# Performance work log

Measured on AMD Instinct MI355X. Metric: run time of the kernel, lower is better.

Reference implementation:

```python
import jax, jax.numpy as jnp
import numpy as np

D_MODEL = 1024
NUM_HEADS = 16
D_K = D_MODEL // NUM_HEADS  # 64
THETA = 10000.0


def setup_inputs() -> dict:
    key = jax.random.key(0)
    k_x, k_q, k_k, k_v, k_o = jax.random.split(key, 5)
    B, S = 2, 2048
    std = (2.0 / (D_MODEL + D_MODEL)) ** 0.5
    x = jax.random.normal(k_x, (B, S, D_MODEL), dtype=jnp.float32)
    Wq = std * jax.random.truncated_normal(k_q, -3.0, 3.0, (D_MODEL, D_MODEL), dtype=jnp.float32)
    Wk = std * jax.random.truncated_normal(k_k, -3.0, 3.0, (D_MODEL, D_MODEL), dtype=jnp.float32)
    Wv = std * jax.random.truncated_normal(k_v, -3.0, 3.0, (D_MODEL, D_MODEL), dtype=jnp.float32)
    Wo = std * jax.random.truncated_normal(k_o, -3.0, 3.0, (D_MODEL, D_MODEL), dtype=jnp.float32)
    return {"x": x, "Wq": Wq, "Wk": Wk, "Wv": Wv, "Wo": Wo}


def _apply_rope(t, cos, sin):
    # t: [B, H, S, d_k]; cos/sin: [S, d_k//2] broadcast over B, H
    tr = t.reshape(*t.shape[:-1], D_K // 2, 2)
    t1, t2 = tr[..., 0], tr[..., 1]
    r1 = t1 * cos - t2 * sin
    r2 = t1 * sin + t2 * cos
    return jnp.stack([r1, r2], axis=-1).reshape(t.shape)


def reference(x, Wq, Wk, Wv, Wo):
    B, S, D = x.shape
    H, dk = NUM_HEADS, D_K
    # projections (no bias): y = x @ W.T
    Q = (x @ Wq.T).reshape(B, S, H, dk).transpose(0, 2, 1, 3)  # [B,H,S,dk]
    K = (x @ Wk.T).reshape(B, S, H, dk).transpose(0, 2, 1, 3)
    V = (x @ Wv.T).reshape(B, S, H, dk).transpose(0, 2, 1, 3)
    # RoPE angles for positions 0..S-1
    pos = jnp.arange(S, dtype=jnp.float32)[:, None]            # [S,1]
    freqs = 1.0 / (THETA ** (jnp.arange(0, dk, 2, dtype=jnp.float32) / dk))  # [dk/2]
    angles = pos * freqs[None, :]                              # [S, dk/2]
    cos, sin = jnp.cos(angles), jnp.sin(angles)
    Q = _apply_rope(Q, cos, sin)
    K = _apply_rope(K, cos, sin)
    # causal scaled dot-product attention
    scores = jnp.einsum("bhqd,bhkd->bhqk", Q, K) / jnp.sqrt(jnp.float32(dk))
    causal = jnp.tril(jnp.ones((S, S), dtype=bool))
    scores = jnp.where(causal, scores, -jnp.inf)
    probs = jax.nn.softmax(scores, axis=-1)
    attn = jnp.einsum("bhqk,bhkd->bhqd", probs, V)             # [B,H,S,dk]
    attn = attn.transpose(0, 2, 1, 3).reshape(B, S, H * dk)
    return attn @ Wo.T
```

## Files before the change

### kernel.cpp

```cpp
#include <hip/hip_runtime.h>
#include <hip/hip_bf16.h>

typedef __bf16 bf16;
typedef __bf16 bf16x8 __attribute__((ext_vector_type(8)));
typedef float f32x4 __attribute__((ext_vector_type(4)));

#define MFMA16(A, B, C) __builtin_amdgcn_mfma_f32_16x16x32_bf16((A), (B), (C), 0, 0, 0)

static __device__ __forceinline__ void gload16(const bf16* g, bf16* l) {
    __builtin_amdgcn_global_load_lds((const __attribute__((address_space(1))) void*)g,
                                     (__attribute__((address_space(3))) void*)l, 16, 0, 0);
}

__global__ void detect_kernel(const void* w, int* flag) {
    float v = (float)((const bf16*)w)[threadIdx.x];
    unsigned long long bad = __ballot(!(fabsf(v) < 1.0f));
    if (threadIdx.x == 0) *flag = bad ? 1 : 0;
}

__global__ __launch_bounds__(256) void convert_all(const void* x, const void* w0,
                                                   const void* w1, const void* w2,
                                                   const void* w3, bf16* xb, bf16* b0,
                                                   bf16* b1, bf16* b2, bf16* b3,
                                                   const int* flagp) {
    if (*flagp == 0) return;
    int id = (blockIdx.x * 256 + threadIdx.x) * 4;
    const int XN = 1 << 22;
    const float* src;
    bf16* dst;
    int off;
    if (id < XN) {
        src = (const float*)x; dst = xb; off = id;
    } else {
        int r = id - XN;
        int wi = r >> 20;
        off = r & ((1 << 20) - 1);
        src = (const float*)(wi == 0 ? w0 : wi == 1 ? w1 : wi == 2 ? w2 : w3);
        dst = (wi == 0 ? b0 : wi == 1 ? b1 : wi == 2 ? b2 : b3);
    }
    float4 v = *(const float4*)(src + off);
    bf16 o[4] = {(bf16)v.x, (bf16)v.y, (bf16)v.z, (bf16)v.w};
    *(uint2*)(dst + off) = *(uint2*)o;
}

__global__ __launch_bounds__(128) void gemm_qkv(const void* rawA, const bf16* convA,
                                                const void* rWq, const bf16* cWq,
                                                const void* rWk, const bf16* cWk,
                                                const void* rWv, const bf16* cWv,
                                                bf16* Qo, bf16* Ko, bf16* Vt,
                                                const int* flagp) {
    const int K = 1024;
    __shared__ __attribute__((aligned(16))) bf16 lsA[128 * 64];
    __shared__ __attribute__((aligned(16))) bf16 lsB[64 * 64];
    const int flag = *flagp;
    const bf16* A = flag ? convA : (const bf16*)rawA;
    const int tensor = blockIdx.x >> 4;
    const int n0 = (blockIdx.x & 15) * 64;
    const bf16* W = tensor == 0 ? (flag ? cWq : (const bf16*)rWq)
                  : tensor == 1 ? (flag ? cWk : (const bf16*)rWk)
                                : (flag ? cWv : (const bf16*)rWv);
    const int t = threadIdx.x;
    const int m0 = blockIdx.y * 128;
    const int w = t >> 6, lane = t & 63;
    const int llo = lane & 15, quad = lane >> 4;
    const int srow = t >> 3;
    const int sc = (t & 7) ^ (srow & 7);
    const bf16* Ab = A + (size_t)(m0 + srow) * K + sc * 8;
    const bf16* Wb = W + (size_t)(n0 + srow) * K + sc * 8;
    bf16* lA = &lsA[t * 8];
    bf16* lB = &lsB[t * 8];

    f32x4 acc[4][4] = {};

    for (int k0 = 0; k0 < K; k0 += 64) {
#pragma unroll
        for (int j = 0; j < 8; ++j) gload16(Ab + (size_t)j * 16 * K + k0, lA + j * 1024);
#pragma unroll
        for (int j = 0; j < 4; ++j) gload16(Wb + (size_t)j * 16 * K + k0, lB + j * 1024);
        __syncthreads();
#pragma unroll
        for (int kc = 0; kc < 2; ++kc) {
            bf16x8 a[4], bb[4];
            const int g = kc * 4 + quad;
#pragma unroll
            for (int mi = 0; mi < 4; ++mi) {
                int r = w * 64 + mi * 16 + llo;
                a[mi] = *(const bf16x8*)&lsA[r * 64 + ((g ^ (r & 7)) * 8)];
            }
#pragma unroll
            for (int ni = 0; ni < 4; ++ni) {
                int r = ni * 16 + llo;
                bb[ni] = *(const bf16x8*)&lsB[r * 64 + ((g ^ (r & 7)) * 8)];
            }
#pragma unroll
            for (int mi = 0; mi < 4; ++mi)
#pragma unroll
                for (int ni = 0; ni < 4; ++ni)
                    acc[mi][ni] = MFMA16(a[mi], bb[ni], acc[mi][ni]);
        }
        __syncthreads();
    }

#pragma unroll
    for (int mi = 0; mi < 4; ++mi)
#pragma unroll
        for (int ni = 0; ni < 4; ++ni)
#pragma unroll
            for (int r = 0; r < 4; ++r) {
                int row = m0 + w * 64 + mi * 16 + quad * 4 + r;
                int col = n0 + ni * 16 + llo;
                float v = acc[mi][ni][r];
                if (tensor == 2) {
                    int b = row >> 11, s = row & 2047;
                    Vt[((size_t)b * 1024 + col) * 2048 + s] = (bf16)v;
                } else {
                    int d = col & 63, s = row & 2047;
                    float partner = __shfl_xor(v, 1);
                    float freq = exp2f((float)(d >> 1) * -0.4152410118609203f);
                    float rev = (float)s * freq * 0.15915494309189535f;
                    rev -= floorf(rev);
                    float sn = __builtin_amdgcn_sinf(rev);
                    float cs = __builtin_amdgcn_cosf(rev);
                    float outv = v * cs + partner * sn * ((d & 1) ? 1.0f : -1.0f);
                    bf16* dst = (tensor == 0) ? Qo : Ko;
                    dst[(size_t)row * 1024 + col] = (bf16)outv;
                }
            }
}

__global__ __launch_bounds__(128) void gemm_out(const bf16* A, const void* rW,
                                                const bf16* cW, void* Cout,
                                                const int* flagp) {
    const int K = 1024, N = 1024;
    __shared__ __attribute__((aligned(16))) bf16 lsA[128 * 64];
    __shared__ __attribute__((aligned(16))) bf16 lsB[64 * 64];
    const int flag = *flagp;
    const bf16* W = flag ? cW : (const bf16*)rW;
    const int t = threadIdx.x;
    const int m0 = blockIdx.y * 128;
    const int n0 = blockIdx.x * 64;
    const int w = t >> 6, lane = t & 63;
    const int llo = lane & 15, quad = lane >> 4;
    const int srow = t >> 3;
    const int sc = (t & 7) ^ (srow & 7);
    const bf16* Ab = A + (size_t)(m0 + srow) * K + sc * 8;
    const bf16* Wb = W + (size_t)(n0 + srow) * K + sc * 8;
    bf16* lA = &lsA[t * 8];
    bf16* lB = &lsB[t * 8];

    f32x4 acc[4][4] = {};

    for (int k0 = 0; k0 < K; k0 += 64) {
#pragma unroll
        for (int j = 0; j < 8; ++j) gload16(Ab + (size_t)j * 16 * K + k0, lA + j * 1024);
#pragma unroll
        for (int j = 0; j < 4; ++j) gload16(Wb + (size_t)j * 16 * K + k0, lB + j * 1024);
        __syncthreads();
#pragma unroll
        for (int kc = 0; kc < 2; ++kc) {
            bf16x8 a[4], bb[4];
            const int g = kc * 4 + quad;
#pragma unroll
            for (int mi = 0; mi < 4; ++mi) {
                int r = w * 64 + mi * 16 + llo;
                a[mi] = *(const bf16x8*)&lsA[r * 64 + ((g ^ (r & 7)) * 8)];
            }
#pragma unroll
            for (int ni = 0; ni < 4; ++ni) {
                int r = ni * 16 + llo;
                bb[ni] = *(const bf16x8*)&lsB[r * 64 + ((g ^ (r & 7)) * 8)];
            }
#pragma unroll
            for (int mi = 0; mi < 4; ++mi)
#pragma unroll
                for (int ni = 0; ni < 4; ++ni)
                    acc[mi][ni] = MFMA16(a[mi], bb[ni], acc[mi][ni]);
        }
        __syncthreads();
    }

#pragma unroll
    for (int mi = 0; mi < 4; ++mi)
#pragma unroll
        for (int ni = 0; ni < 4; ++ni)
#pragma unroll
            for (int r = 0; r < 4; ++r) {
                int row = m0 + w * 64 + mi * 16 + quad * 4 + r;
                int col = n0 + ni * 16 + llo;
                float v = acc[mi][ni][r];
                if (flag)
                    ((float*)Cout)[(size_t)row * N + col] = v;
                else
                    ((bf16*)Cout)[(size_t)row * N + col] = (bf16)v;
            }
}

__global__ __launch_bounds__(256) void attn_kernel(const bf16* __restrict__ Q,
                                                   const bf16* __restrict__ Kr,
                                                   const bf16* __restrict__ Vt,
                                                   bf16* __restrict__ O) {
    __shared__ __attribute__((aligned(16))) bf16 lsK[64 * 64];
    __shared__ __attribute__((aligned(16))) bf16 lsV[64 * 64];
    __shared__ __attribute__((aligned(16))) bf16 lsP[4][16 * 72];
    const int blk = blockIdx.x;
    const int ib = 31 - (blk >> 5);
    const int bh = blk & 31;
    const int b = bh >> 4, h = bh & 15;
    const int t = threadIdx.x, w = t >> 6, lane = t & 63;
    const int llo = lane & 15, quad = lane >> 4;
    const int q0 = ib * 64 + w * 16;

    const size_t qbase = ((size_t)(b * 2048 + q0 + llo)) * 1024 + h * 64 + quad * 8;
    bf16x8 aQ0 = *(const bf16x8*)&Q[qbase];
    bf16x8 aQ1 = *(const bf16x8*)&Q[qbase + 32];

    f32x4 o[4] = {};
    float lpart[4] = {0.f, 0.f, 0.f, 0.f};
    const float SC = 0.18033688011112042f;
    const int qrow = q0 + quad * 4;

    const int srow8 = lane >> 3;
    const int sc = (lane & 7) ^ srow8;

    for (int tt = 0; tt <= ib; ++tt) {
        const int kv0 = tt * 64;
#pragma unroll
        for (int jj = 0; jj < 2; ++jj) {
            int seg = w + jj * 4;
            int rowk = seg * 8 + srow8;
            gload16(&Kr[((size_t)(b * 2048 + kv0 + rowk)) * 1024 + h * 64 + sc * 8],
                    &lsK[seg * 512 + lane * 8]);
            gload16(&Vt[((size_t)(b * 1024 + h * 64 + rowk)) * 2048 + kv0 + sc * 8],
                    &lsV[seg * 512 + lane * 8]);
        }
        __syncthreads();
        f32x4 s[4];
#pragma unroll
        for (int half = 0; half < 4; ++half) {
            int rk = half * 16 + llo;
            bf16x8 k0 = *(const bf16x8*)&lsK[rk * 64 + ((quad ^ (rk & 7)) * 8)];
            bf16x8 k1 = *(const bf16x8*)&lsK[rk * 64 + (((quad + 4) ^ (rk & 7)) * 8)];
            f32x4 z = {};
            z = MFMA16(aQ0, k0, z);
            z = MFMA16(aQ1, k1, z);
            s[half] = z;
        }
        if (tt == ib) {
#pragma unroll
            for (int half = 0; half < 4; ++half) {
                int kv = kv0 + half * 16 + llo;
#pragma unroll
                for (int r = 0; r < 4; ++r) {
                    float e = (kv <= qrow + r) ? s[half][r] * SC : -INFINITY;
                    float p = exp2f(e);
                    lpart[r] += p;
                    lsP[w][(quad * 4 + r) * 72 + half * 16 + llo] = (bf16)p;
                }
            }
        } else {
#pragma unroll
            for (int half = 0; half < 4; ++half)
#pragma unroll
                for (int r = 0; r < 4; ++r) {
                    float p = exp2f(s[half][r] * SC);
                    lpart[r] += p;
                    lsP[w][(quad * 4 + r) * 72 + half * 16 + llo] = (bf16)p;
                }
        }
        __builtin_amdgcn_wave_barrier();
#pragma unroll
        for (int kc = 0; kc < 2; ++kc) {
            bf16x8 aP = *(const bf16x8*)&lsP[w][llo * 72 + kc * 32 + quad * 8];
#pragma unroll
            for (int g = 0; g < 4; ++g) {
                int rv = g * 16 + llo;
                int cg = kc * 4 + quad;
                bf16x8 bV = *(const bf16x8*)&lsV[rv * 64 + ((cg ^ (rv & 7)) * 8)];
                o[g] = MFMA16(aP, bV, o[g]);
            }
        }
        __syncthreads();
    }

#pragma unroll
    for (int r = 0; r < 4; ++r) {
        float l = lpart[r];
#pragma unroll
        for (int off = 1; off < 16; off <<= 1) l += __shfl_xor(l, off);
        float inv = 1.f / l;
        size_t ob = ((size_t)(b * 2048 + q0 + quad * 4 + r)) * 1024 + h * 64;
#pragma unroll
        for (int g = 0; g < 4; ++g) O[ob + g * 16 + llo] = (bf16)(o[g][r] * inv);
    }
}

extern "C" void kernel_launch(void* const* d_in, const int* in_sizes, int n_in,
                              void* d_out, int out_size, void* d_ws, size_t ws_size,
                              hipStream_t stream) {
    const size_t TN = (size_t)4096 * 1024;

    int* flag = (int*)d_ws;
    bf16* Q = (bf16*)((char*)d_ws + 256);
    bf16* Kb = Q + TN;
    bf16* Vt = Kb + TN;
    bf16* xb = Vt + TN;
    bf16* Wb0 = xb + TN;
    bf16* Wb1 = Wb0 + TN / 4;
    bf16* Wb2 = Wb1 + TN / 4;
    bf16* Wb3 = Wb2 + TN / 4;
    bf16* AO = Q;

    detect_kernel<<<1, 64, 0, stream>>>(d_in[1], flag);
    convert_all<<<8192, 256, 0, stream>>>(d_in[0], d_in[1], d_in[2], d_in[3], d_in[4],
                                          xb, Wb0, Wb1, Wb2, Wb3, flag);

    gemm_qkv<<<dim3(48, 32), 128, 0, stream>>>(d_in[0], xb, d_in[1], Wb0, d_in[2], Wb1,
                                               d_in[3], Wb2, Q, Kb, Vt, flag);

    attn_kernel<<<1024, 256, 0, stream>>>(Q, Kb, Vt, AO);

    gemm_out<<<dim3(16, 32), 128, 0, stream>>>(AO, d_in[4], Wb3, d_out, flag);
}
```

Measured before the change: 209.8 us.

## Enlarge GEMM tiles to 128x128 and give attention waves 32 query rows

The QKV and output projections now share one templated GEMM using 128x128 tiles with four waves, halving the number of B-tile loads per output. The attention kernel processes 128 queries per block (32 per wave), computing scores in transposed form and storing probabilities with packed writes, and skips fully-masked KV chunks per wave. This raises operand reuse from LDS for K/V but halves the block counts, which can reduce occupancy and increase causal load imbalance.

New measurement: 227.9 us. 1.09x slower.

```diff
diff --git a/kernel.cpp b/kernel.cpp
--- a/kernel.cpp
+++ b/kernel.cpp
@@ -43,26 +43,37 @@
     *(uint2*)(dst + off) = *(uint2*)o;
 }
 
-__global__ __launch_bounds__(128) void gemm_qkv(const void* rawA, const bf16* convA,
-                                                const void* rWq, const bf16* cWq,
-                                                const void* rWk, const bf16* cWk,
-                                                const void* rWv, const bf16* cWv,
-                                                bf16* Qo, bf16* Ko, bf16* Vt,
-                                                const int* flagp) {
+template <int MODE>
+__global__ __launch_bounds__(256) void gemm128(const void* rawA, const bf16* convA,
+                                               const void* rW0, const bf16* cW0,
+                                               const void* rW1, const bf16* cW1,
+                                               const void* rW2, const bf16* cW2,
+                                               bf16* Qo, bf16* Ko, bf16* Vt,
+                                               void* Cout, const int* flagp) {
     const int K = 1024;
     __shared__ __attribute__((aligned(16))) bf16 lsA[128 * 64];
-    __shared__ __attribute__((aligned(16))) bf16 lsB[64 * 64];
+    __shared__ __attribute__((aligned(16))) bf16 lsB[128 * 64];
     const int flag = *flagp;
     const bf16* A = flag ? convA : (const bf16*)rawA;
-    const int tensor = blockIdx.x >> 4;
-    const int n0 = (blockIdx.x & 15) * 64;
-    const bf16* W = tensor == 0 ? (flag ? cWq : (const bf16*)rWq)
-                  : tensor == 1 ? (flag ? cWk : (const bf16*)rWk)
-                                : (flag ? cWv : (const bf16*)rWv);
+    int tensor, n0;
+    const bf16* W;
+    if (MODE == 0) {
+        tensor = blockIdx.x >> 3;
+        n0 = (blockIdx.x & 7) * 128;
+        W = tensor == 0 ? (flag ? cW0 : (const bf16*)rW0)
+          : tensor == 1 ? (flag ? cW1 : (const bf16*)rW1)
+                        : (flag ? cW2 : (const bf16*)rW2);
+    } else {
+        tensor = 0;
+        n0 = blockIdx.x * 128;
+        W = flag ? cW0 : (const bf16*)rW0;
+    }
     const int t = threadIdx.x;
     const int m0 = blockIdx.y * 128;
     const int w = t >> 6, lane = t & 63;
+    const int wr = w >> 1, wc = w & 1;
     const int llo = lane & 15, quad = lane >> 4;
+
     const int srow = t >> 3;
     const int sc = (t & 7) ^ (srow & 7);
     const bf16* Ab = A + (size_t)(m0 + srow) * K + sc * 8;
@@ -74,9 +85,9 @@
 
     for (int k0 = 0; k0 < K; k0 += 64) {
 #pragma unroll
-        for (int j = 0; j < 8; ++j) gload16(Ab + (size_t)j * 16 * K + k0, lA + j * 1024);
-#pragma unroll
-        for (int j = 0; j < 4; ++j) gload16(Wb + (size_t)j * 16 * K + k0, lB + j * 1024);
+        for (int j = 0; j < 4; ++j) gload16(Ab + (size_t)j * 32 * K + k0, lA + j * 2048);
+#pragma unroll
+        for (int j = 0; j < 4; ++j) gload16(Wb + (size_t)j * 32 * K + k0, lB + j * 2048);
         __syncthreads();
 #pragma unroll
         for (int kc = 0; kc < 2; ++kc) {
@@ -84,12 +95,12 @@
             const int g = kc * 4 + quad;
 #pragma unroll
             for (int mi = 0; mi < 4; ++mi) {
-                int r = w * 64 + mi * 16 + llo;
+                int r = wr * 64 + mi * 16 + llo;
                 a[mi] = *(const bf16x8*)&lsA[r * 64 + ((g ^ (r & 7)) * 8)];
             }
 #pragma unroll
             for (int ni = 0; ni < 4; ++ni) {
-                int r = ni * 16 + llo;
+                int r = wc * 64 + ni * 16 + llo;
                 bb[ni] = *(const bf16x8*)&lsB[r * 64 + ((g ^ (r & 7)) * 8)];
             }
 #pragma unroll
@@ -107,10 +118,15 @@
         for (int ni = 0; ni < 4; ++ni)
 #pragma unroll
             for (int r = 0; r < 4; ++r) {
-                int row = m0 + w * 64 + mi * 16 + quad * 4 + r;
-                int col = n0 + ni * 16 + llo;
+                int row = m0 + wr * 64 + mi * 16 + quad * 4 + r;
+                int col = n0 + wc * 64 + ni * 16 + llo;
                 float v = acc[mi][ni][r];
-                if (tensor == 2) {
+                if (MODE == 1) {
+                    if (flag)
+                        ((float*)Cout)[(size_t)row * 1024 + col] = v;
+                    else
+                        ((bf16*)Cout)[(size_t)row * 1024 + col] = (bf16)v;
+                } else if (tensor == 2) {
                     int b = row >> 11, s = row & 2047;
                     Vt[((size_t)b * 1024 + col) * 2048 + s] = (bf16)v;
                 } else {
@@ -128,101 +144,39 @@
             }
 }
 
-__global__ __launch_bounds__(128) void gemm_out(const bf16* A, const void* rW,
-                                                const bf16* cW, void* Cout,
-                                                const int* flagp) {
-    const int K = 1024, N = 1024;
-    __shared__ __attribute__((aligned(16))) bf16 lsA[128 * 64];
-    __shared__ __attribute__((aligned(16))) bf16 lsB[64 * 64];
-    const int flag = *flagp;
-    const bf16* W = flag ? cW : (const bf16*)rW;
-    const int t = threadIdx.x;
-    const int m0 = blockIdx.y * 128;
-    const int n0 = blockIdx.x * 64;
-    const int w = t >> 6, lane = t & 63;
-    const int llo = lane & 15, quad = lane >> 4;
-    const int srow = t >> 3;
-    const int sc = (t & 7) ^ (srow & 7);
-    const bf16* Ab = A + (size_t)(m0 + srow) * K + sc * 8;
-    const bf16* Wb = W + (size_t)(n0 + srow) * K + sc * 8;
-    bf16* lA = &lsA[t * 8];
-    bf16* lB = &lsB[t * 8];
-
-    f32x4 acc[4][4] = {};
-
-    for (int k0 = 0; k0 < K; k0 += 64) {
-#pragma unroll
-        for (int j = 0; j < 8; ++j) gload16(Ab + (size_t)j * 16 * K + k0, lA + j * 1024);
-#pragma unroll
-        for (int j = 0; j < 4; ++j) gload16(Wb + (size_t)j * 16 * K + k0, lB + j * 1024);
-        __syncthreads();
-#pragma unroll
-        for (int kc = 0; kc < 2; ++kc) {
-            bf16x8 a[4], bb[4];
-            const int g = kc * 4 + quad;
-#pragma unroll
-            for (int mi = 0; mi < 4; ++mi) {
-                int r = w * 64 + mi * 16 + llo;
-                a[mi] = *(const bf16x8*)&lsA[r * 64 + ((g ^ (r & 7)) * 8)];
-            }
-#pragma unroll
-            for (int ni = 0; ni < 4; ++ni) {
-                int r = ni * 16 + llo;
-                bb[ni] = *(const bf16x8*)&lsB[r * 64 + ((g ^ (r & 7)) * 8)];
-            }
-#pragma unroll
-            for (int mi = 0; mi < 4; ++mi)
-#pragma unroll
-                for (int ni = 0; ni < 4; ++ni)
-                    acc[mi][ni] = MFMA16(a[mi], bb[ni], acc[mi][ni]);
-        }
-        __syncthreads();
-    }
-
-#pragma unroll
-    for (int mi = 0; mi < 4; ++mi)
-#pragma unroll
-        for (int ni = 0; ni < 4; ++ni)
-#pragma unroll
-            for (int r = 0; r < 4; ++r) {
-                int row = m0 + w * 64 + mi * 16 + quad * 4 + r;
-                int col = n0 + ni * 16 + llo;
-                float v = acc[mi][ni][r];
-                if (flag)
-                    ((float*)Cout)[(size_t)row * N + col] = v;
-                else
-                    ((bf16*)Cout)[(size_t)row * N + col] = (bf16)v;
-            }
-}
-
 __global__ __launch_bounds__(256) void attn_kernel(const bf16* __restrict__ Q,
                                                    const bf16* __restrict__ Kr,
                                                    const bf16* __restrict__ Vt,
                                                    bf16* __restrict__ O) {
     __shared__ __attribute__((aligned(16))) bf16 lsK[64 * 64];
     __shared__ __attribute__((aligned(16))) bf16 lsV[64 * 64];
-    __shared__ __attribute__((aligned(16))) bf16 lsP[4][16 * 72];
+    __shared__ __attribute__((aligned(16))) bf16 lsP[4][32 * 72];
     const int blk = blockIdx.x;
-    const int ib = 31 - (blk >> 5);
+    const int ib = 15 - (blk >> 5);
     const int bh = blk & 31;
     const int b = bh >> 4, h = bh & 15;
     const int t = threadIdx.x, w = t >> 6, lane = t & 63;
     const int llo = lane & 15, quad = lane >> 4;
-    const int q0 = ib * 64 + w * 16;
-
-    const size_t qbase = ((size_t)(b * 2048 + q0 + llo)) * 1024 + h * 64 + quad * 8;
-    bf16x8 aQ0 = *(const bf16x8*)&Q[qbase];
-    bf16x8 aQ1 = *(const bf16x8*)&Q[qbase + 32];
-
-    f32x4 o[4] = {};
-    float lpart[4] = {0.f, 0.f, 0.f, 0.f};
+    const int Q0 = ib * 128, q0w = Q0 + w * 32;
+
+    bf16x8 aQ[2][2];
+#pragma unroll
+    for (int qi = 0; qi < 2; ++qi) {
+        const size_t qb = ((size_t)(b * 2048 + q0w + qi * 16 + llo)) * 1024 + h * 64 + quad * 8;
+        aQ[qi][0] = *(const bf16x8*)&Q[qb];
+        aQ[qi][1] = *(const bf16x8*)&Q[qb + 32];
+    }
+
+    f32x4 o[2][4] = {};
+    float lpart[2] = {0.f, 0.f};
     const float SC = 0.18033688011112042f;
-    const int qrow = q0 + quad * 4;
+    const int qlane0 = q0w + llo;
 
     const int srow8 = lane >> 3;
     const int sc = (lane & 7) ^ srow8;
-
-    for (int tt = 0; tt <= ib; ++tt) {
+    const int nch = 2 * ib + 2;
+
+    for (int tt = 0; tt < nch; ++tt) {
         const int kv0 = tt * 64;
 #pragma unroll
         for (int jj = 0; jj < 2; ++jj) {
@@ -234,64 +188,81 @@
                     &lsV[seg * 512 + lane * 8]);
         }
         __syncthreads();
-        f32x4 s[4];
-#pragma unroll
-        for (int half = 0; half < 4; ++half) {
-            int rk = half * 16 + llo;
-            bf16x8 k0 = *(const bf16x8*)&lsK[rk * 64 + ((quad ^ (rk & 7)) * 8)];
-            bf16x8 k1 = *(const bf16x8*)&lsK[rk * 64 + (((quad + 4) ^ (rk & 7)) * 8)];
-            f32x4 z = {};
-            z = MFMA16(aQ0, k0, z);
-            z = MFMA16(aQ1, k1, z);
-            s[half] = z;
-        }
-        if (tt == ib) {
-#pragma unroll
-            for (int half = 0; half < 4; ++half) {
-                int kv = kv0 + half * 16 + llo;
-#pragma unroll
-                for (int r = 0; r < 4; ++r) {
-                    float e = (kv <= qrow + r) ? s[half][r] * SC : -INFINITY;
-                    float p = exp2f(e);
-                    lpart[r] += p;
-                    lsP[w][(quad * 4 + r) * 72 + half * 16 + llo] = (bf16)p;
+
+        if (kv0 <= q0w + 31) {
+            const bool need_mask = (kv0 + 63 >= q0w);
+#pragma unroll
+            for (int qi = 0; qi < 2; ++qi) {
+                const int q = qlane0 + qi * 16;
+#pragma unroll
+                for (int half = 0; half < 4; ++half) {
+                    int rk = half * 16 + llo;
+                    bf16x8 k0 = *(const bf16x8*)&lsK[rk * 64 + ((quad ^ (rk & 7)) * 8)];
+                    bf16x8 k1 = *(const bf16x8*)&lsK[rk * 64 + (((quad + 4) ^ (rk & 7)) * 8)];
+                    f32x4 z = {};
+                    z = MFMA16(k0, aQ[qi][0], z);
+                    z = MFMA16(k1, aQ[qi][1], z);
+                    union { bf16 hh[4]; uint2 u; } pk;
+                    if (need_mask) {
+                        int kvb = kv0 + half * 16 + quad * 4;
+#pragma unroll
+                        for (int r = 0; r < 4; ++r) {
+                            float e = (kvb + r <= q) ? z[r] * SC : -INFINITY;
+                            float p = exp2f(e);
+                            lpart[qi] += p;
+                            pk.hh[r] = (bf16)p;
+                        }
+                    } else {
+#pragma unroll
+                        for (int r = 0; r < 4; ++r) {
+                            float p = exp2f(z[r] * SC);
+                            lpart[qi] += p;
+                            pk.hh[r] = (bf16)p;
+                        }
+                    }
+                    *(uint2*)&lsP[w][(qi * 16 + llo) * 72 + half * 16 + quad * 4] = pk.u;
                 }
             }
-        } else {
-#pragma unroll
-            for (int half = 0; half < 4; ++half)
-#pragma unroll
-                for (int r = 0; r < 4; ++r) {
-                    float p = exp2f(s[half][r] * SC);
-                    lpart[r] += p;
-                    lsP[w][(quad * 4 + r) * 72 + half * 16 + llo] = (bf16)p;
+            __builtin_amdgcn_wave_barrier();
+#pragma unroll
+            for (int qi = 0; qi < 2; ++qi)
+#pragma unroll
+                for (int kc = 0; kc < 2; ++kc) {
+                    bf16x8 aP =
+                        *(const bf16x8*)&lsP[w][(qi * 16 + llo) * 72 + kc * 32 + quad * 8];
+#pragma unroll
+                    for (int g = 0; g < 4; ++g) {
+                        int rv = g * 16 + llo;
+                        int cg = kc * 4 + quad;
+                        bf16x8 bV = *(const bf16x8*)&lsV[rv * 64 + ((cg ^ (rv & 7)) * 8)];
+                        o[qi][g] = MFMA16(aP, bV, o[qi][g]);
+                    }
                 }
-        }
-        __builtin_amdgcn_wave_barrier();
-#pragma unroll
-        for (int kc = 0; kc < 2; ++kc) {
-            bf16x8 aP = *(const bf16x8*)&lsP[w][llo * 72 + kc * 32 + quad * 8];
-#pragma unroll
-            for (int g = 0; g < 4; ++g) {
-                int rv = g * 16 + llo;
-                int cg = kc * 4 + quad;
-                bf16x8 bV = *(const bf16x8*)&lsV[rv * 64 + ((cg ^ (rv & 7)) * 8)];
-                o[g] = MFMA16(aP, bV, o[g]);
-            }
-        }
-        __syncthreads();
-    }
-
-#pragma unroll
-    for (int r = 0; r < 4; ++r) {
-        float l = lpart[r];
-#pragma unroll
-        for (int off = 1; off < 16; off <<= 1) l += __shfl_xor(l, off);
-        float inv = 1.f / l;
-        size_t ob = ((size_t)(b * 2048 + q0 + quad * 4 + r)) * 1024 + h * 64;
-#pragma unroll
-        for (int g = 0; g < 4; ++g) O[ob + g * 16 + llo] = (bf16)(o[g][r] * inv);
-    }
+            __builtin_amdgcn_wave_barrier();
+        }
+        __syncthreads();
+    }
+
+    float lfull[2];
+#pragma unroll
+    for (int qi = 0; qi < 2; ++qi) {
+        float l = lpart[qi];
+        l += __shfl_xor(l, 16);
+        l += __shfl_xor(l, 32);
+        lfull[qi] = l;
+    }
+#pragma unroll
+    for (int qi = 0; qi < 2; ++qi)
+#pragma unroll
+        for (int r = 0; r < 4; ++r) {
+            float l = __shfl(lfull[qi], (lane & 48) | (quad * 4 + r));
+            float inv = 1.f / l;
+            int q = q0w + qi * 16 + quad * 4 + r;
+            size_t ob = ((size_t)(b * 2048 + q)) * 1024 + h * 64;
+#pragma unroll
+            for (int g = 0; g < 4; ++g)
+                O[ob + g * 16 + llo] = (bf16)(o[qi][g][r] * inv);
+        }
 }
 
 extern "C" void kernel_launch(void* const* d_in, const int* in_sizes, int n_in,
@@ -314,10 +285,13 @@
     convert_all<<<8192, 256, 0, stream>>>(d_in[0], d_in[1], d_in[2], d_in[3], d_in[4],
                                           xb, Wb0, Wb1, Wb2, Wb3, flag);
 
-    gemm_qkv<<<dim3(48, 32), 128, 0, stream>>>(d_in[0], xb, d_in[1], Wb0, d_in[2], Wb1,
-                                               d_in[3], Wb2, Q, Kb, Vt, flag);
-
-    attn_kernel<<<1024, 256, 0, stream>>>(Q, Kb, Vt, AO);
-
-    gemm_out<<<dim3(16, 32), 128, 0, stream>>>(AO, d_in[4], Wb3, d_out, flag);
-}
+    gemm128<0><<<dim3(24, 32), 256, 0, stream>>>(d_in[0], xb, d_in[1], Wb0, d_in[2],
+                                                 Wb1, d_in[3], Wb2, Q, Kb, Vt, nullptr,
+                                                 flag);
+
+    attn_kernel<<<512, 256, 0, stream>>>(Q, Kb, Vt, AO);
+
+    gemm128<1><<<dim3(8, 32), 256, 0, stream>>>(AO, AO, d_in[4], Wb3, nullptr, nullptr,
+                                                nullptr, nullptr, nullptr, nullptr,
+                                                nullptr, d_out, flag);
+}
```
